# Performance work log

Hardware: AMD Instinct MI355X
Metric: run time of the kernel (lower is better)

## Reference

```python
import jax, jax.numpy as jnp
import numpy as np

B, T, N, H = 32, 512, 32, 128  # batch, time, num_series (== num_chans), hidden


def setup_inputs() -> dict:
    key = jax.random.key(0)
    ks = jax.random.split(key, 7)
    s = 1.0 / np.sqrt(H)  # PyTorch LSTM default init range
    X = jax.random.normal(ks[0], (B, T, N), dtype=jnp.float32)
    W_ih = jax.random.uniform(ks[1], (N, 4 * H, N), minval=-s, maxval=s, dtype=jnp.float32)
    W_hh = jax.random.uniform(ks[2], (N, 4 * H, H), minval=-s, maxval=s, dtype=jnp.float32)
    b_ih = jax.random.uniform(ks[3], (N, 4 * H), minval=-s, maxval=s, dtype=jnp.float32)
    b_hh = jax.random.uniform(ks[4], (N, 4 * H), minval=-s, maxval=s, dtype=jnp.float32)
    W_out = jax.random.uniform(ks[5], (N, H), minval=-s, maxval=s, dtype=jnp.float32)  # Conv1d(hidden,1,1) weight per series
    b_out = jax.random.uniform(ks[6], (N,), minval=-s, maxval=s, dtype=jnp.float32)
    return dict(X=X, W_ih=W_ih, W_hh=W_hh, b_ih=b_ih, b_hh=b_hh, W_out=W_out, b_out=b_out)


def reference(X, W_ih, W_hh, b_ih, b_hh, W_out, b_out):
    """Ensemble of N independent single-layer LSTMs over the same input X,
    each followed by a 1x1 conv (linear) head; outputs concatenated on dim 2.
    Gate order follows PyTorch: i, f, g, o."""
    Bsz, Tlen, P = X.shape
    Nser, _, Hid = W_hh.shape
    # Precompute input projections for all series/timesteps: [T, N, B, 4H]
    xproj = jnp.einsum('btp,ngp->tnbg', X, W_ih) + (b_ih + b_hh)[None, :, None, :]
    h0 = jnp.zeros((Nser, Bsz, Hid), X.dtype)
    c0 = jnp.zeros((Nser, Bsz, Hid), X.dtype)

    def step(carry, xt):
        h, c = carry
        gates = xt + jnp.einsum('nbh,ngh->nbg', h, W_hh)  # [N,B,4H]
        i, f, g, o = jnp.split(gates, 4, axis=-1)
        c = jax.nn.sigmoid(f) * c + jax.nn.sigmoid(i) * jnp.tanh(g)
        h = jax.nn.sigmoid(o) * jnp.tanh(c)
        return (h, c), h

    (hT, cT), hs = jax.lax.scan(step, (h0, c0), xproj)  # hs: [T, N, B, H]
    # 1x1 conv head per series, then concatenate along series dim -> [B, T, N]
    pred = jnp.einsum('tnbh,nh->btn', hs, W_out) + b_out[None, None, :]
    return pred, hT, cT
```

## Files before the change

kernel.cpp:

```cpp
#include <hip/hip_runtime.h>
#include <hip/hip_bf16.h>

typedef __attribute__((ext_vector_type(8))) short s16x8;
typedef __attribute__((ext_vector_type(4))) float f32x4;

#define MFMA_B16(a, b, c) __builtin_amdgcn_mfma_f32_16x16x32_bf16((a), (b), (c), 0, 0, 0)

static __device__ __forceinline__ short f2bf(float f) {
    __hip_bfloat16 h = __float2bfloat16(f);
    return __builtin_bit_cast(short, h);
}
static __device__ __forceinline__ float rcp_f(float x) {
    return __builtin_amdgcn_rcpf(x);
}

__global__ void xcvt_kernel(const float* __restrict__ X, short* __restrict__ Xb, int n) {
    int i = (blockIdx.x * 256 + threadIdx.x) * 4;
    if (i < n) {
        float4 v = *(const float4*)(X + i);
        short4 o;
        o.x = f2bf(v.x); o.y = f2bf(v.y); o.z = f2bf(v.z); o.w = f2bf(v.w);
        *(short4*)(Xb + i) = o;
    }
}

template<bool BF16X>
__global__ __launch_bounds__(512, 2)
void clstm_kernel(const float* __restrict__ X,
                  const short* __restrict__ Xb,
                  const float* __restrict__ W_ih,
                  const float* __restrict__ W_hh,
                  const float* __restrict__ b_ih,
                  const float* __restrict__ b_hh,
                  const float* __restrict__ W_out,
                  const float* __restrict__ b_out,
                  float* __restrict__ out)
{
    constexpr int B = 32, T = 512, N = 32, H = 128, G = 512;
    constexpr int HT_OFF = B * T * N;
    constexpr int CT_OFF = HT_OFF + N * B * H;
    constexpr int PRED_OFF = 8192;
    constexpr float C1  = 1.4426950408889634f;
    constexpr float C2  = 2.8853900817779268f;
    constexpr float CFX = -0.34657359027997264f;

    __shared__ __align__(16) unsigned char smem[16384];

    const int tid  = threadIdx.x;
    const int w    = tid >> 6;
    const int L    = tid & 63;
    const int col  = L & 15;
    const int quad = L >> 4;
    const int n    = blockIdx.x & 31;
    const int bgrp = blockIdx.x >> 5;

    s16x8 Bh[4][4];
    s16x8 Bx[4];
    f32x4 biasv[4];
#pragma unroll
    for (int tt = 0; tt < 4; ++tt) {
        const float s_tt = (tt == 2) ? -C2 : -C1;
        const int g = (w + 8 * tt) * 16 + col;
        const float* whr = W_hh + ((size_t)n * G + g) * H + quad * 8;
#pragma unroll
        for (int kt = 0; kt < 4; ++kt) {
            const float* p = whr + kt * 32;
#pragma unroll
            for (int jj = 0; jj < 8; ++jj) Bh[tt][kt][jj] = f2bf(s_tt * p[jj]);
        }
        const float* wir = W_ih + ((size_t)n * G + g) * N + quad * 8;
#pragma unroll
        for (int jj = 0; jj < 8; ++jj) Bx[tt][jj] = f2bf(s_tt * wir[jj]);
        const float bb = s_tt * (b_ih[n * G + g] + b_hh[n * G + g]);
        biasv[tt] = (f32x4){bb, bb, bb, bb};
    }

    s16x8 Bp[4];
    const float bo = b_out[n];
    const f32x4 bov = (f32x4){bo, bo, bo, bo};
#pragma unroll
    for (int kt = 0; kt < 4; ++kt) {
        const float* wp = W_out + n * H + kt * 32 + quad * 8;
#pragma unroll
        for (int jj = 0; jj < 8; ++jj)
            Bp[kt][jj] = (col == 0) ? f2bf(wp[jj]) : (short)0;
    }

    int wboff;
    {
        const int j = w * 16 + col;
        wboff = (j >> 5) * 1024 + (((((j >> 3) & 3) << 4) | (quad << 2)) * 16) + (j & 7) * 2;
    }

    const int xb = bgrp * 4 + (col >> 2);
    const int ts = col & 3;
    const float* xp  = X + ((size_t)xb * T + ts) * N + quad * 8;
    const short* xbp = BF16X ? (Xb + ((size_t)xb * T + ts) * N + quad * 8) : nullptr;

    auto loadxg = [&](int tg) -> s16x8 {
        if constexpr (BF16X) {
            return *(const s16x8*)(xbp + (size_t)tg * N);
        } else {
            float4 lo = *(const float4*)(xp + (size_t)tg * N);
            float4 hi = *(const float4*)(xp + (size_t)tg * N + 4);
            s16x8 r;
            r[0] = f2bf(lo.x); r[1] = f2bf(lo.y); r[2] = f2bf(lo.z); r[3] = f2bf(lo.w);
            r[4] = f2bf(hi.x); r[5] = f2bf(hi.y); r[6] = f2bf(hi.z); r[7] = f2bf(hi.w);
            return r;
        }
    };

    *(float4*)(smem + tid * 16)        = make_float4(0.f, 0.f, 0.f, 0.f);
    *(float4*)(smem + 8192 + tid * 16) = make_float4(0.f, 0.f, 0.f, 0.f);

    float cstp = 0.f, hlast = 0.f;

    s16x8 xgC = loadxg(0);
    s16x8 xgN = loadxg(4);

    __syncthreads();

#define STEP(P, TCUR, J)                                                            \
    {                                                                               \
        const unsigned char* rb = smem + (P) * 4096;                                \
        s16x8 Af[4];                                                                \
        _Pragma("unroll")                                                           \
        for (int kt = 0; kt < 4; ++kt)                                              \
            Af[kt] = *(const s16x8*)(rb + kt * 1024 + L * 16);                      \
        f32x4 cur[4];                                                               \
        _Pragma("unroll")                                                           \
        for (int tt = 0; tt < 4; ++tt)                                              \
            cur[tt] = MFMA_B16(Af[0], Bh[tt][0], acc4[tt]);                         \
        _Pragma("unroll")                                                           \
        for (int kt = 1; kt < 4; ++kt) {                                            \
            _Pragma("unroll")                                                       \
            for (int tt = 0; tt < 4; ++tt)                                          \
                cur[tt] = MFMA_B16(Af[kt], Bh[tt][kt], cur[tt]);                    \
        }                                                                           \
        if (w == ((TCUR) & 7)) {                                                    \
            f32x4 pacc = bov;                                                       \
            _Pragma("unroll")                                                       \
            for (int kt = 0; kt < 4; ++kt)                                          \
                pacc = MFMA_B16(Af[kt], Bp[kt], pacc);                              \
            if ((TCUR) > 0 && col == 0)                                             \
                *(float*)(smem + PRED_OFF + ((quad << 9) + (TCUR) - 1) * 4) =       \
                    pacc[0];                                                        \
        }                                                                           \
                     \
        {                                                                           \
            const float iv = cur[0][(J)], fv = cur[1][(J)];                         \
            const float gv = cur[2][(J)], ov = cur[3][(J)];                         \
            const float ei = exp2f(iv);                                             \
            const float ef = exp2f(fv);                                             \
            const float eg = exp2f(gv);                                             \
            const float eo = exp2f(ov);                                             \
            const float sf  = rcp_f(1.0f + ef);                                     \
            const float tgm = __builtin_fmaf(C2, eg, -C2);                          \
            const float itgp = tgm * rcp_f((1.0f + ei) * (1.0f + eg));              \
            const float ccp = __builtin_fmaf(sf, cstp, itgp);                       \
            cstp = ccp;                                                             \
            const float ec = exp2f(ccp);                                            \
            const float hv = (1.0f - ec) * rcp_f((1.0f + eo) * (1.0f + ec));        \
            hlast = hv;                                                             \
            const short hb = f2bf(hv);                                              \
            unsigned char* wbp = smem + ((P) ^ 1) * 4096 + wboff;                   \
            *(short*)(wbp)      = hb;                                               \
            *(short*)(wbp + 16) = hb;                                               \
            *(short*)(wbp + 32) = hb;                                               \
            *(short*)(wbp + 48) = hb;                                               \
        }                                                                           \
        __syncthreads();                                                            \
    }

#pragma unroll 1
    for (int tg = 0; tg < T; tg += 4) {
        f32x4 acc4[4];
#pragma unroll
        for (int tt = 0; tt < 4; ++tt)
            acc4[tt] = MFMA_B16(xgC, Bx[tt], biasv[tt]);
        xgC = xgN;
        xgN = loadxg((tg + 8 < T) ? (tg + 8) : (T - 4));
        STEP(0, tg + 0, 0)
        STEP(1, tg + 1, 1)
        STEP(0, tg + 2, 2)
        STEP(1, tg + 3, 3)
    }
#undef STEP

    if (w == 0) {
        f32x4 pacc = bov;
#pragma unroll
        for (int kt = 0; kt < 4; ++kt) {
            s16x8 Af = *(const s16x8*)(smem + kt * 1024 + L * 16);
            pacc = MFMA_B16(Af, Bp[kt], pacc);
        }
        if (col == 0)
            *(float*)(smem + PRED_OFF + ((quad << 9) + (T - 1)) * 4) = pacc[0];
    }
    __syncthreads();

#pragma unroll
    for (int e = tid; e < 4 * T; e += 512) {
        const int b = e >> 9, t = e & (T - 1);
        out[((size_t)(bgrp * 4 + b) * T + t) * N + n] =
            *(const float*)(smem + PRED_OFF + e * 4);
    }

    {
        const int bglob = bgrp * 4 + quad;
        const int j = w * 16 + col;
        out[HT_OFF + ((size_t)n * B + bglob) * H + j] = hlast;
        out[CT_OFF + ((size_t)n * B + bglob) * H + j] = cstp * CFX;
    }
}

extern "C" void kernel_launch(void* const* d_in, const int* in_sizes, int n_in,
                              void* d_out, int out_size, void* d_ws, size_t ws_size,
                              hipStream_t stream) {
    const float* X     = (const float*)d_in[0];
    const float* W_ih  = (const float*)d_in[1];
    const float* W_hh  = (const float*)d_in[2];
    const float* b_ih  = (const float*)d_in[3];
    const float* b_hh  = (const float*)d_in[4];
    const float* W_out = (const float*)d_in[5];
    const float* b_out = (const float*)d_in[6];
    float* out = (float*)d_out;

    const int xelems = 32 * 512 * 32;
    const bool usebf = ws_size >= (size_t)xelems * sizeof(short);

    if (usebf) {
        short* Xb = (short*)d_ws;
        xcvt_kernel<<<dim3(xelems / 1024), dim3(256), 0, stream>>>(X, Xb, xelems);
        clstm_kernel<true><<<dim3(256), dim3(512), 0, stream>>>(
            X, Xb, W_ih, W_hh, b_ih, b_hh, W_out, b_out, out);
    } else {
        clstm_kernel<false><<<dim3(256), dim3(512), 0, stream>>>(
            X, nullptr, W_ih, W_hh, b_ih, b_hh, W_out, b_out, out);
    }
}
```

Measured before the change: 341.5 us.

## Halve batch rows per block and double grid for two blocks per CU

Each block now handles 2 batch rows instead of 4, and the grid doubles to 512 blocks. Two independent latency-bound recurrence chains can then share each CU and hide each other's MFMA, LDS and barrier latency. To make room in registers, the bias vectors and output-projection weights move from registers into a larger LDS buffer and are re-read every step. The cost is half-wasted MFMA rows, duplicated weight setup per block, and extra LDS traffic inside the serial loop.

```diff
diff --git a/kernel.cpp b/kernel.cpp
--- a/kernel.cpp
+++ b/kernel.cpp
@@ -40,11 +40,13 @@
     constexpr int HT_OFF = B * T * N;
     constexpr int CT_OFF = HT_OFF + N * B * H;
     constexpr int PRED_OFF = 8192;
+    constexpr int BP_OFF   = 12288;
+    constexpr int BV_OFF   = 16384;
     constexpr float C1  = 1.4426950408889634f;
     constexpr float C2  = 2.8853900817779268f;
     constexpr float CFX = -0.34657359027997264f;
 
-    __shared__ __align__(16) unsigned char smem[16384];
+    __shared__ __align__(16) unsigned char smem[49152];
 
     const int tid  = threadIdx.x;
     const int w    = tid >> 6;
@@ -56,7 +58,6 @@
 
     s16x8 Bh[4][4];
     s16x8 Bx[4];
-    f32x4 biasv[4];
 #pragma unroll
     for (int tt = 0; tt < 4; ++tt) {
         const float s_tt = (tt == 2) ? -C2 : -C1;
@@ -72,18 +73,22 @@
 #pragma unroll
         for (int jj = 0; jj < 8; ++jj) Bx[tt][jj] = f2bf(s_tt * wir[jj]);
         const float bb = s_tt * (b_ih[n * G + g] + b_hh[n * G + g]);
-        biasv[tt] = (f32x4){bb, bb, bb, bb};
-    }
-
-    s16x8 Bp[4];
+        *(f32x4*)(smem + BV_OFF + tt * 8192 + tid * 16) = (f32x4){bb, bb, bb, bb};
+    }
+
+    if (tid < 256) *(float4*)(smem + BP_OFF + tid * 16) = make_float4(0.f, 0.f, 0.f, 0.f);
     const float bo = b_out[n];
-    const f32x4 bov = (f32x4){bo, bo, bo, bo};
-#pragma unroll
-    for (int kt = 0; kt < 4; ++kt) {
-        const float* wp = W_out + n * H + kt * 32 + quad * 8;
-#pragma unroll
-        for (int jj = 0; jj < 8; ++jj)
-            Bp[kt][jj] = (col == 0) ? f2bf(wp[jj]) : (short)0;
+    *(float4*)(smem + tid * 16) = make_float4(0.f, 0.f, 0.f, 0.f);
+    __syncthreads();
+    if (col == 0) {
+#pragma unroll
+        for (int kt = 0; kt < 4; ++kt) {
+            s16x8 f;
+            const float* wp = W_out + n * H + kt * 32 + quad * 8;
+#pragma unroll
+            for (int jj = 0; jj < 8; ++jj) f[jj] = f2bf(wp[jj]);
+            *(s16x8*)(smem + BP_OFF + kt * 1024 + L * 16) = f;
+        }
     }
 
     int wboff;
@@ -91,8 +96,9 @@
         const int j = w * 16 + col;
         wboff = (j >> 5) * 1024 + (((((j >> 3) & 3) << 4) | (quad << 2)) * 16) + (j & 7) * 2;
     }
-
-    const int xb = bgrp * 4 + (col >> 2);
+    const bool cellactive = (quad < 2);
+
+    const int xb = bgrp * 2 + ((col >> 2) & 1);
     const int ts = col & 3;
     const float* xp  = X + ((size_t)xb * T + ts) * N + quad * 8;
     const short* xbp = BF16X ? (Xb + ((size_t)xb * T + ts) * N + quad * 8) : nullptr;
@@ -109,9 +115,6 @@
             return r;
         }
     };
-
-    *(float4*)(smem + tid * 16)        = make_float4(0.f, 0.f, 0.f, 0.f);
-    *(float4*)(smem + 8192 + tid * 16) = make_float4(0.f, 0.f, 0.f, 0.f);
 
     float cstp = 0.f, hlast = 0.f;
 
@@ -138,13 +141,15 @@
                 cur[tt] = MFMA_B16(Af[kt], Bh[tt][kt], cur[tt]);                    \
         }                                                                           \
         if (w == ((TCUR) & 7)) {                                                    \
-            f32x4 pacc = bov;                                                       \
+            f32x4 pacc = (f32x4){0.f, 0.f, 0.f, 0.f};                               \
             _Pragma("unroll")                                                       \
-            for (int kt = 0; kt < 4; ++kt)                                          \
-                pacc = MFMA_B16(Af[kt], Bp[kt], pacc);                              \
-            if ((TCUR) > 0 && col == 0)                                             \
+            for (int kt = 0; kt < 4; ++kt) {                                        \
+                s16x8 Bpk = *(const s16x8*)(smem + BP_OFF + kt * 1024 + L * 16);    \
+                pacc = MFMA_B16(Af[kt], Bpk, pacc);                                 \
+            }                                                                       \
+            if ((TCUR) > 0 && col == 0 && cellactive)                               \
                 *(float*)(smem + PRED_OFF + ((quad << 9) + (TCUR) - 1) * 4) =       \
-                    pacc[0];                                                        \
+                    pacc[0] + bo;                                                   \
         }                                                                           \
                      \
         {                                                                           \
@@ -176,8 +181,10 @@
     for (int tg = 0; tg < T; tg += 4) {
         f32x4 acc4[4];
 #pragma unroll
-        for (int tt = 0; tt < 4; ++tt)
-            acc4[tt] = MFMA_B16(xgC, Bx[tt], biasv[tt]);
+        for (int tt = 0; tt < 4; ++tt) {
+            const f32x4 bv = *(const f32x4*)(smem + BV_OFF + tt * 8192 + tid * 16);
+            acc4[tt] = MFMA_B16(xgC, Bx[tt], bv);
+        }
         xgC = xgN;
         xgN = loadxg((tg + 8 < T) ? (tg + 8) : (T - 4));
         STEP(0, tg + 0, 0)
@@ -188,26 +195,27 @@
 #undef STEP
 
     if (w == 0) {
-        f32x4 pacc = bov;
+        f32x4 pacc = (f32x4){0.f, 0.f, 0.f, 0.f};
 #pragma unroll
         for (int kt = 0; kt < 4; ++kt) {
             s16x8 Af = *(const s16x8*)(smem + kt * 1024 + L * 16);
-            pacc = MFMA_B16(Af, Bp[kt], pacc);
-        }
-        if (col == 0)
-            *(float*)(smem + PRED_OFF + ((quad << 9) + (T - 1)) * 4) = pacc[0];
+            s16x8 Bpk = *(const s16x8*)(smem + BP_OFF + kt * 1024 + L * 16);
+            pacc = MFMA_B16(Af, Bpk, pacc);
+        }
+        if (col == 0 && cellactive)
+            *(float*)(smem + PRED_OFF + ((quad << 9) + (T - 1)) * 4) = pacc[0] + bo;
     }
     __syncthreads();
 
 #pragma unroll
-    for (int e = tid; e < 4 * T; e += 512) {
+    for (int e = tid; e < 2 * T; e += 512) {
         const int b = e >> 9, t = e & (T - 1);
-        out[((size_t)(bgrp * 4 + b) * T + t) * N + n] =
+        out[((size_t)(bgrp * 2 + b) * T + t) * N + n] =
             *(const float*)(smem + PRED_OFF + e * 4);
     }
 
-    {
-        const int bglob = bgrp * 4 + quad;
+    if (cellactive) {
+        const int bglob = bgrp * 2 + quad;
         const int j = w * 16 + col;
         out[HT_OFF + ((size_t)n * B + bglob) * H + j] = hlast;
         out[CT_OFF + ((size_t)n * B + bglob) * H + j] = cstp * CFX;
@@ -232,10 +240,10 @@
     if (usebf) {
         short* Xb = (short*)d_ws;
         xcvt_kernel<<<dim3(xelems / 1024), dim3(256), 0, stream>>>(X, Xb, xelems);
-        clstm_kernel<true><<<dim3(256), dim3(512), 0, stream>>>(
+        clstm_kernel<true><<<dim3(512), dim3(512), 0, stream>>>(
             X, Xb, W_ih, W_hh, b_ih, b_hh, W_out, b_out, out);
     } else {
-        clstm_kernel<false><<<dim3(256), dim3(512), 0, stream>>>(
+        clstm_kernel<false><<<dim3(512), dim3(512), 0, stream>>>(
             X, nullptr, W_ih, W_hh, b_ih, b_hh, W_out, b_out, out);
     }
 }
```

Measured after the change: 630.9 us. 84.8% more time.
